# Kernel tuning notes

Hardware: AMD Instinct MI355X
Metric: run time of the kernel (lower is better)

## Reference

```python
import jax, jax.numpy as jnp
import numpy as np

UNITS = 128
N_CLASSES = 10
N_FEAT = 3
R_ON = 0.05      # time-gate open ratio
ALPHA = 0.001    # leak during closed phase
LN_EPS = 1e-3    # keras LayerNormalization default epsilon


def _time_gate(t, tau, s):
    # t: [B], tau/s: [U] -> k: [B, U]
    phi = jnp.mod(t[:, None] - s, tau) / tau
    k = jnp.where(phi < 0.5 * R_ON, 2.0 * phi / R_ON,
        jnp.where(phi < R_ON, 2.0 - 2.0 * phi / R_ON, ALPHA * phi))
    return k


def _plstm_step(x, t, h, c, Wx, Wh, b, tau, s):
    z = x @ Wx + h @ Wh + b                      # [B, 4U]
    i, f, g, o = jnp.split(z, 4, axis=-1)
    c_hat = jax.nn.sigmoid(f) * c + jax.nn.sigmoid(i) * jnp.tanh(g)
    h_hat = jax.nn.sigmoid(o) * jnp.tanh(c_hat)
    k = _time_gate(t, tau, s)
    return k * h_hat + (1.0 - k) * h, k * c_hat + (1.0 - k) * c


def _layer_norm(x, gamma, beta):
    mu = jnp.mean(x, axis=-1, keepdims=True)
    var = jnp.mean(jnp.square(x - mu), axis=-1, keepdims=True)
    return gamma * (x - mu) * jax.lax.rsqrt(var + LN_EPS) + beta


def setup_inputs() -> dict:
    key = jax.random.key(0)
    ks = jax.random.split(key, 16)
    B, T, F, U, C = 256, 1000, N_FEAT, UNITS, N_CLASSES
    inputs = jax.random.normal(ks[0], (B, T, F), dtype=jnp.float32)
    # strictly increasing-ish observation times per sequence
    times = jnp.cumsum(jax.random.uniform(ks[1], (B, T), dtype=jnp.float32), axis=1)
    sc_in = 1.0 / np.sqrt(F)
    sc_h = 1.0 / np.sqrt(U)
    Wx0 = jax.random.normal(ks[2], (F, 4 * U), dtype=jnp.float32) * sc_in
    Wh0 = jax.random.normal(ks[3], (U, 4 * U), dtype=jnp.float32) * sc_h
    b0 = jnp.zeros((4 * U,), dtype=jnp.float32)
    tau0 = jnp.exp(jax.random.uniform(ks[4], (U,), minval=0.0, maxval=3.0, dtype=jnp.float32))
    s0 = jax.random.uniform(ks[5], (U,), dtype=jnp.float32) * tau0
    Wx1 = jax.random.normal(ks[6], (U, 4 * U), dtype=jnp.float32) * sc_h
    Wh1 = jax.random.normal(ks[7], (U, 4 * U), dtype=jnp.float32) * sc_h
    b1 = jnp.zeros((4 * U,), dtype=jnp.float32)
    tau1 = jnp.exp(jax.random.uniform(ks[8], (U,), minval=0.0, maxval=3.0, dtype=jnp.float32))
    s1 = jax.random.uniform(ks[9], (U,), dtype=jnp.float32) * tau1
    gamma = jnp.ones((U,), dtype=jnp.float32)
    beta = jnp.zeros((U,), dtype=jnp.float32)
    Wfc = jax.random.normal(ks[10], (U, C), dtype=jnp.float32) * sc_h
    bfc = jnp.zeros((C,), dtype=jnp.float32)
    return {"inputs": inputs, "times": times, "Wx0": Wx0, "Wh0": Wh0, "b0": b0,
            "tau0": tau0, "s0": s0, "Wx1": Wx1, "Wh1": Wh1, "b1": b1,
            "tau1": tau1, "s1": s1, "gamma": gamma, "beta": beta,
            "Wfc": Wfc, "bfc": bfc}


def reference(inputs, times, Wx0, Wh0, b0, tau0, s0, Wx1, Wh1, b1, tau1, s1,
              gamma, beta, Wfc, bfc):
    B, T, F = inputs.shape
    U = Wh0.shape[0]
    x_t = jnp.transpose(inputs, (1, 0, 2))   # [T, B, F]
    t_t = jnp.transpose(times, (1, 0))       # [T, B]

    def step(carry, xt):
        h0, c0, h1, c1 = carry
        x, t = xt
        h0, c0 = _plstm_step(x, t, h0, c0, Wx0, Wh0, b0, tau0, s0)
        hn = _layer_norm(h0, gamma, beta)
        h1, c1 = _plstm_step(hn, t, h1, c1, Wx1, Wh1, b1, tau1, s1)
        probs = jax.nn.softmax(h1 @ Wfc + bfc, axis=-1)
        return (h0, c0, h1, c1), probs

    zeros = jnp.zeros((B, U), dtype=inputs.dtype)
    init = (zeros, zeros, zeros, zeros)
    _, out = jax.lax.scan(step, init, (x_t, t_t))  # out: [T, B, C]
    return jnp.transpose(out, (1, 0, 2))           # [B, T, C]
```

## Files before the change

### kernel.cpp

```cpp
#include <hip/hip_runtime.h>
#include <math.h>

constexpr int U      = 128;
constexpr int G4     = 512;
constexpr int NCls   = 10;
constexpr int TSTEPS = 1000;
constexpr int BATCH  = 256;
constexpr int CROWS  = 48;


__device__ __forceinline__ float sigm(float x) {
    return 1.0f / (1.0f + __expf(-x));
}

__device__ __forceinline__ float tgate(float t, float tau, float s) {
    float r = fmodf(t - s, tau);
    if (r < 0.0f) r += tau;
    const float phi = r / tau;
    return (phi < 0.025f) ? 40.0f * phi
         : (phi < 0.05f)  ? 2.0f - 40.0f * phi
         : 0.001f * phi;
}

#define ROW4(WP, I, HB) { \
    float4 w_; \
    w_ = (WP)[((I)+0)*128]; ac.x += (HB).x*w_.x; ac.y += (HB).x*w_.y; ac.z += (HB).x*w_.z; ac.w += (HB).x*w_.w; \
    w_ = (WP)[((I)+1)*128]; ac.x += (HB).y*w_.x; ac.y += (HB).y*w_.y; ac.z += (HB).y*w_.z; ac.w += (HB).y*w_.w; \
    w_ = (WP)[((I)+2)*128]; ac.x += (HB).z*w_.x; ac.y += (HB).z*w_.y; ac.z += (HB).z*w_.z; ac.w += (HB).z*w_.w; \
    w_ = (WP)[((I)+3)*128]; ac.x += (HB).w*w_.x; ac.y += (HB).w*w_.y; ac.z += (HB).w*w_.z; ac.w += (HB).w*w_.w; }

__global__ __launch_bounds__(1024, 1) void plstm_fused(
    const float* __restrict__ inputs,
    const float* __restrict__ times,
    const float* __restrict__ Wx0,
    const float* __restrict__ Wh0,
    const float* __restrict__ b0,
    const float* __restrict__ tau0,
    const float* __restrict__ s0,
    const float* __restrict__ Wx1,
    const float* __restrict__ Wh1,
    const float* __restrict__ b1,
    const float* __restrict__ tau1,
    const float* __restrict__ s1,
    const float* __restrict__ gamma_,
    const float* __restrict__ beta_,
    const float* __restrict__ Wfc,
    const float* __restrict__ bfc,
    float* __restrict__ out)
{
    const int tid = threadIdx.x;
    const int c4  = tid & 127;
    const int g   = tid >> 7;
    const int b   = blockIdx.x;

    __shared__ __align__(16) float wh0c[CROWS * G4];
    __shared__ __align__(16) float zu[8 * G4];
    __shared__ __align__(16) float h0s[U];
    __shared__ __align__(16) float ghu[2 * U];
    __shared__ __align__(16) float b0s[G4], b1s[G4], Ps[G4], Qs[G4];
    __shared__ __align__(16) float wx0s[3 * G4];
    __shared__ __align__(16) float wfcs[U * 11];
    __shared__ float bfcs[NCls];
    __shared__ float red[4];
    __shared__ float gms[U], bts[U];

    if (tid < U) { gms[tid] = gamma_[tid]; bts[tid] = beta_[tid];
                   h0s[tid] = 0.f; ghu[tid] = 0.f; ghu[U + tid] = 0.f; }
    {
        float4* dst = reinterpret_cast<float4*>(wh0c);
        const float4* src = reinterpret_cast<const float4*>(Wh0);
        #pragma unroll
        for (int i = 0; i < 6; ++i) dst[tid + i * 1024] = src[tid + i * 1024];
    }
    if (tid < G4) { b0s[tid] = b0[tid]; b1s[tid] = b1[tid]; }
    for (int i = tid; i < 3 * G4; i += 1024) wx0s[i] = Wx0[i];
    for (int i = tid; i < U * NCls; i += 1024) {
        const int u = i / NCls, c = i - u * NCls;
        wfcs[u * 11 + c] = Wfc[i];
    }
    if (tid < NCls) bfcs[tid] = bfc[tid];
    __syncthreads();

    if (tid < G4) {
        float P = 0.f, Q = 0.f;
        #pragma unroll 8
        for (int u = 0; u < U; ++u) {
            const float w = Wx1[u * G4 + tid];
            Q += gms[u] * w;
            P += bts[u] * w;
        }
        Ps[tid] = P; Qs[tid] = Q;
    }

    float tau0r = 0.f, s0r = 0.f, tau1r = 0.f, s1r = 0.f, gr = 0.f;
    if (tid < U) {
        tau0r = tau0[tid]; s0r = s0[tid];
        tau1r = tau1[tid]; s1r = s1[tid];
        gr = gms[tid];
    }
    float c0r = 0.f, c1r = 0.f, h0r = 0.f, h1r = 0.f;

    const float* __restrict__ xp = inputs + (size_t)b * TSTEPS * 3;
    const float* __restrict__ tp = times  + (size_t)b * TSTEPS;
    float*       __restrict__ op = out    + (size_t)b * TSTEPS * NCls;

    float xa0 = xp[0], xa1 = xp[1], xa2 = xp[2], tva = tp[0];

    __syncthreads();

    for (int t = 0; t < TSTEPS; ++t) {
        const float x0 = xa0, x1 = xa1, x2 = xa2, tv = tva;
        const int tn = (t + 1 < TSTEPS) ? t + 1 : t;
        xa0 = xp[tn*3+0]; xa1 = xp[tn*3+1]; xa2 = xp[tn*3+2]; tva = tp[tn];

        {
            float4 ac = make_float4(0.f, 0.f, 0.f, 0.f);
            const int r0 = g * 16;
            if (g < 3) {
                const float4* wp = reinterpret_cast<const float4*>(wh0c) + r0 * 128 + c4;
                #pragma unroll 2
                for (int i = 0; i < 16; i += 4) {
                    const float4 hb = *reinterpret_cast<const float4*>(&h0s[r0 + i]);
                    ROW4(wp, i, hb);
                }
            } else {
                const float4* wp = reinterpret_cast<const float4*>(Wh0) + r0 * 128 + c4;
                #pragma unroll 2
                for (int i = 0; i < 16; i += 4) {
                    const float4 hb = *reinterpret_cast<const float4*>(&h0s[r0 + i]);
                    ROW4(wp, i, hb);
                }
            }
            *reinterpret_cast<float4*>(&zu[g * G4 + 4 * c4]) = ac;
        }
        __syncthreads();

        if (tid < U) {
            const int u = tid;
            float z[4];
            #pragma unroll
            for (int q = 0; q < 4; ++q) {
                const int c = u + q * 128;
                float s = b0s[c] + x0 * wx0s[c] + x1 * wx0s[G4 + c] + x2 * wx0s[2 * G4 + c];
                #pragma unroll
                for (int gg = 0; gg < 8; ++gg) s += zu[gg * G4 + c];
                z[q] = s;
            }
            const float ig = sigm(z[0]);
            const float fg = sigm(z[1]);
            const float gg = tanhf(z[2]);
            const float og = sigm(z[3]);
            const float ch = fg * c0r + ig * gg;
            const float hh = og * tanhf(ch);
            const float k  = tgate(tv, tau0r, s0r);
            const float hn = k * hh + (1.0f - k) * h0r;
            c0r = k * ch + (1.0f - k) * c0r;
            h0r = hn;
            h0s[u] = hn;
            ghu[u] = gr * hn;
            float ssum = hn, qsum = hn * hn;
            #pragma unroll
            for (int off = 1; off < 64; off <<= 1) {
                ssum += __shfl_xor(ssum, off);
                qsum += __shfl_xor(qsum, off);
            }
            if ((tid & 63) == 0) {
                red[(tid >> 6) * 2]     = ssum;
                red[(tid >> 6) * 2 + 1] = qsum;
            }
        }
        __syncthreads();

        {
            const int half = tid >> 9;
            const int rg   = (tid >> 7) & 3;
            const int r0   = rg * 32;
            const float* __restrict__ Wm = half ? Wh1 : Wx1;
            const float* hvp = ghu + half * U + r0;
            const float4* wp = reinterpret_cast<const float4*>(Wm) + r0 * 128 + c4;
            float4 ac = make_float4(0.f, 0.f, 0.f, 0.f);
            #pragma unroll 2
            for (int i = 0; i < 32; i += 4) {
                const float4 hb = *reinterpret_cast<const float4*>(&hvp[i]);
                ROW4(wp, i, hb);
            }
            *reinterpret_cast<float4*>(&zu[(half * 4 + rg) * G4 + 4 * c4]) = ac;
        }
        __syncthreads();

        if (tid < U) {
            const float mu    = (red[0] + red[2]) * (1.0f / 128.0f);
            const float msq   = (red[1] + red[3]) * (1.0f / 128.0f);
            const float rstd  = rsqrtf(msq - mu * mu + 1e-3f);
            const float murstd = mu * rstd;
            const int u = tid;
            float z[4];
            #pragma unroll
            for (int q = 0; q < 4; ++q) {
                const int c = u + q * 128;
                const float sx = (zu[0*G4+c] + zu[1*G4+c]) + (zu[2*G4+c] + zu[3*G4+c]);
                const float sh = (zu[4*G4+c] + zu[5*G4+c]) + (zu[6*G4+c] + zu[7*G4+c]);
                z[q] = b1s[c] + Ps[c] + rstd * sx - murstd * Qs[c] + sh;
            }
            const float ig = sigm(z[0]);
            const float fg = sigm(z[1]);
            const float gg = tanhf(z[2]);
            const float og = sigm(z[3]);
            const float ch = fg * c1r + ig * gg;
            const float hh = og * tanhf(ch);
            const float k  = tgate(tv, tau1r, s1r);
            const float hn = k * hh + (1.0f - k) * h1r;
            c1r = k * ch + (1.0f - k) * c1r;
            h1r = hn;
            ghu[U + u] = hn;
        }
        __syncthreads();

        if (tid < 64) {
            const float a  = ghu[U + tid];
            const float bv = ghu[U + tid + 64];
            float p[NCls];
            #pragma unroll
            for (int c = 0; c < NCls; ++c)
                p[c] = a * wfcs[tid * 11 + c] + bv * wfcs[(tid + 64) * 11 + c];
            #pragma unroll
            for (int off = 1; off < 64; off <<= 1) {
                #pragma unroll
                for (int c = 0; c < NCls; ++c) p[c] += __shfl_xor(p[c], off);
            }
            float m = -1e30f;
            #pragma unroll
            for (int c = 0; c < NCls; ++c) { p[c] += bfcs[c]; m = fmaxf(m, p[c]); }
            float ssum = 0.0f;
            #pragma unroll
            for (int c = 0; c < NCls; ++c) { p[c] = __expf(p[c] - m); ssum += p[c]; }
            const float inv = 1.0f / ssum;
            float pv = p[0];
            #pragma unroll
            for (int c = 1; c < NCls; ++c) if (tid == c) pv = p[c];
            if (tid < NCls) op[t * NCls + tid] = pv * inv;
        }
    }
}

extern "C" void kernel_launch(void* const* d_in, const int* in_sizes, int n_in,
                              void* d_out, int out_size, void* d_ws, size_t ws_size,
                              hipStream_t stream) {
    const float* inputs = (const float*)d_in[0];
    const float* times  = (const float*)d_in[1];
    const float* Wx0    = (const float*)d_in[2];
    const float* Wh0    = (const float*)d_in[3];
    const float* b0     = (const float*)d_in[4];
    const float* tau0   = (const float*)d_in[5];
    const float* s0     = (const float*)d_in[6];
    const float* Wx1    = (const float*)d_in[7];
    const float* Wh1    = (const float*)d_in[8];
    const float* b1     = (const float*)d_in[9];
    const float* tau1   = (const float*)d_in[10];
    const float* s1     = (const float*)d_in[11];
    const float* gamma_ = (const float*)d_in[12];
    const float* beta_  = (const float*)d_in[13];
    const float* Wfc    = (const float*)d_in[14];
    const float* bfc    = (const float*)d_in[15];
    float* out = (float*)d_out;

    dim3 grid(BATCH);
    dim3 block(1024);
    hipLaunchKernelGGL(plstm_fused, grid, block, 0, stream,
                       inputs, times, Wx0, Wh0, b0, tau0, s0,
                       Wx1, Wh1, b1, tau1, s1, gamma_, beta_, Wfc, bfc, out);
}
```

Before: 7.087 ms.

## Halve block size and keep part of recurrent weights in registers

The block shrinks from 1024 to 512 threads. Each thread now holds 12 rows of Wh0 and 4 rows of Wx1/Wh1 as float4 registers. The rest of Wh0 is split between shared memory and global/L2 streaming, and the layer-1 matvec is regrouped into 4 partial sums instead of 8, which cuts the number of partial-sum reductions. Time-gate parameters move to shared memory to save registers. The aim is less shared and global weight traffic per timestep, at the cost of more serial FMA work per thread and higher register pressure with half the threads.

Measured after the change: 6.842 ms. 3.5% less time.

```diff
diff --git a/kernel.cpp b/kernel.cpp
--- a/kernel.cpp
+++ b/kernel.cpp
@@ -6,7 +6,6 @@
 constexpr int NCls   = 10;
 constexpr int TSTEPS = 1000;
 constexpr int BATCH  = 256;
-constexpr int CROWS  = 48;
 
 
 __device__ __forceinline__ float sigm(float x) {
@@ -29,7 +28,13 @@
     w_ = (WP)[((I)+2)*128]; ac.x += (HB).z*w_.x; ac.y += (HB).z*w_.y; ac.z += (HB).z*w_.z; ac.w += (HB).z*w_.w; \
     w_ = (WP)[((I)+3)*128]; ac.x += (HB).w*w_.x; ac.y += (HB).w*w_.y; ac.z += (HB).w*w_.z; ac.w += (HB).w*w_.w; }
 
-__global__ __launch_bounds__(1024, 1) void plstm_fused(
+#define ROW4P(W0, W1, W2, W3, HB) { \
+    ac.x += (HB).x*(W0).x; ac.y += (HB).x*(W0).y; ac.z += (HB).x*(W0).z; ac.w += (HB).x*(W0).w; \
+    ac.x += (HB).y*(W1).x; ac.y += (HB).y*(W1).y; ac.z += (HB).y*(W1).z; ac.w += (HB).y*(W1).w; \
+    ac.x += (HB).z*(W2).x; ac.y += (HB).z*(W2).y; ac.z += (HB).z*(W2).z; ac.w += (HB).z*(W2).w; \
+    ac.x += (HB).w*(W3).x; ac.y += (HB).w*(W3).y; ac.z += (HB).w*(W3).z; ac.w += (HB).w*(W3).w; }
+
+__global__ __launch_bounds__(512, 1) void plstm_fused(
     const float* __restrict__ inputs,
     const float* __restrict__ times,
     const float* __restrict__ Wx0,
@@ -53,35 +58,48 @@
     const int g   = tid >> 7;
     const int b   = blockIdx.x;
 
-    __shared__ __align__(16) float wh0c[CROWS * G4];
-    __shared__ __align__(16) float zu[8 * G4];
+    __shared__ __align__(16) float wh0c[48 * G4];
+    __shared__ __align__(16) float zuA[4 * G4];
+    __shared__ __align__(16) float zuB[4 * G4];
     __shared__ __align__(16) float h0s[U];
     __shared__ __align__(16) float ghu[2 * U];
     __shared__ __align__(16) float b0s[G4], b1s[G4], Ps[G4], Qs[G4];
     __shared__ __align__(16) float wx0s[3 * G4];
     __shared__ __align__(16) float wfcs[U * 11];
+    __shared__ float tau0s[U], s0s[U], tau1s[U], s1s[U];
     __shared__ float bfcs[NCls];
     __shared__ float red[4];
     __shared__ float gms[U], bts[U];
 
-    if (tid < U) { gms[tid] = gamma_[tid]; bts[tid] = beta_[tid];
-                   h0s[tid] = 0.f; ghu[tid] = 0.f; ghu[U + tid] = 0.f; }
+    if (tid < U) {
+        gms[tid] = gamma_[tid]; bts[tid] = beta_[tid];
+        tau0s[tid] = tau0[tid]; s0s[tid] = s0[tid];
+        tau1s[tid] = tau1[tid]; s1s[tid] = s1[tid];
+        h0s[tid] = 0.f; ghu[tid] = 0.f; ghu[U + tid] = 0.f;
+    }
     {
         float4* dst = reinterpret_cast<float4*>(wh0c);
-        const float4* src = reinterpret_cast<const float4*>(Wh0);
         #pragma unroll
-        for (int i = 0; i < 6; ++i) dst[tid + i * 1024] = src[tid + i * 1024];
+        for (int i = 0; i < 12; ++i) {
+            const int idx  = i * 512 + tid;
+            const int slot = idx >> 7;
+            const int cq   = idx & 127;
+            const int grp  = slot / 12;
+            const int row  = 32 * grp + 12 + (slot - grp * 12);
+            dst[slot * 128 + cq] =
+                *reinterpret_cast<const float4*>(&Wh0[row * G4 + 4 * cq]);
+        }
     }
     if (tid < G4) { b0s[tid] = b0[tid]; b1s[tid] = b1[tid]; }
-    for (int i = tid; i < 3 * G4; i += 1024) wx0s[i] = Wx0[i];
-    for (int i = tid; i < U * NCls; i += 1024) {
+    for (int i = tid; i < 3 * G4; i += 512) wx0s[i] = Wx0[i];
+    for (int i = tid; i < U * NCls; i += 512) {
         const int u = i / NCls, c = i - u * NCls;
         wfcs[u * 11 + c] = Wfc[i];
     }
     if (tid < NCls) bfcs[tid] = bfc[tid];
     __syncthreads();
 
-    if (tid < G4) {
+    {
         float P = 0.f, Q = 0.f;
         #pragma unroll 8
         for (int u = 0; u < U; ++u) {
@@ -92,13 +110,26 @@
         Ps[tid] = P; Qs[tid] = Q;
     }
 
-    float tau0r = 0.f, s0r = 0.f, tau1r = 0.f, s1r = 0.f, gr = 0.f;
-    if (tid < U) {
-        tau0r = tau0[tid]; s0r = s0[tid];
-        tau1r = tau1[tid]; s1r = s1[tid];
-        gr = gms[tid];
-    }
-    float c0r = 0.f, c1r = 0.f, h0r = 0.f, h1r = 0.f;
+    float4 wh0r[12];
+    #pragma unroll
+    for (int i = 0; i < 12; ++i)
+        wh0r[i] = *reinterpret_cast<const float4*>(&Wh0[(32 * g + i) * G4 + 4 * c4]);
+    const float* __restrict__ Wc = (g < 2) ? Wx1 : Wh1;
+    const int rb = 64 * (g & 1);
+    float4 wcr[4];
+    #pragma unroll
+    for (int i = 0; i < 4; ++i)
+        wcr[i] = *reinterpret_cast<const float4*>(&Wc[(rb + i) * G4 + 4 * c4]);
+
+    float c0r = 0.f, h0r = 0.f, c1r = 0.f, h1r = 0.f;
+
+    const float4* __restrict__ wlA =
+        reinterpret_cast<const float4*>(wh0c) + (12 * g) * 128 + c4;
+    const float4* __restrict__ wsA =
+        reinterpret_cast<const float4*>(Wh0) + (32 * g + 24) * 128 + c4;
+    const float4* __restrict__ wsC =
+        reinterpret_cast<const float4*>(Wc) + (rb + 4) * 128 + c4;
+    const float* __restrict__ hvC = ghu + 64 * g;
 
     const float* __restrict__ xp = inputs + (size_t)b * TSTEPS * 3;
     const float* __restrict__ tp = times  + (size_t)b * TSTEPS;
@@ -115,23 +146,25 @@
 
         {
             float4 ac = make_float4(0.f, 0.f, 0.f, 0.f);
-            const int r0 = g * 16;
-            if (g < 3) {
-                const float4* wp = reinterpret_cast<const float4*>(wh0c) + r0 * 128 + c4;
-                #pragma unroll 2
-                for (int i = 0; i < 16; i += 4) {
-                    const float4 hb = *reinterpret_cast<const float4*>(&h0s[r0 + i]);
-                    ROW4(wp, i, hb);
-                }
-            } else {
-                const float4* wp = reinterpret_cast<const float4*>(Wh0) + r0 * 128 + c4;
-                #pragma unroll 2
-                for (int i = 0; i < 16; i += 4) {
-                    const float4 hb = *reinterpret_cast<const float4*>(&h0s[r0 + i]);
-                    ROW4(wp, i, hb);
-                }
-            }
-            *reinterpret_cast<float4*>(&zu[g * G4 + 4 * c4]) = ac;
+            {
+                const float4 hb0 = *reinterpret_cast<const float4*>(&h0s[32 * g + 0]);
+                ROW4P(wh0r[0], wh0r[1], wh0r[2], wh0r[3], hb0);
+                const float4 hb1 = *reinterpret_cast<const float4*>(&h0s[32 * g + 4]);
+                ROW4P(wh0r[4], wh0r[5], wh0r[6], wh0r[7], hb1);
+                const float4 hb2 = *reinterpret_cast<const float4*>(&h0s[32 * g + 8]);
+                ROW4P(wh0r[8], wh0r[9], wh0r[10], wh0r[11], hb2);
+            }
+            #pragma unroll
+            for (int i = 0; i < 12; i += 4) {
+                const float4 hb = *reinterpret_cast<const float4*>(&h0s[32 * g + 12 + i]);
+                ROW4(wlA, i, hb);
+            }
+            #pragma unroll
+            for (int i = 0; i < 8; i += 4) {
+                const float4 hb = *reinterpret_cast<const float4*>(&h0s[32 * g + 24 + i]);
+                ROW4(wsA, i, hb);
+            }
+            *reinterpret_cast<float4*>(&zuA[g * G4 + 4 * c4]) = ac;
         }
         __syncthreads();
 
@@ -142,22 +175,19 @@
             for (int q = 0; q < 4; ++q) {
                 const int c = u + q * 128;
                 float s = b0s[c] + x0 * wx0s[c] + x1 * wx0s[G4 + c] + x2 * wx0s[2 * G4 + c];
-                #pragma unroll
-                for (int gg = 0; gg < 8; ++gg) s += zu[gg * G4 + c];
+                s += (zuA[c] + zuA[G4 + c]) + (zuA[2 * G4 + c] + zuA[3 * G4 + c]);
                 z[q] = s;
             }
-            const float ig = sigm(z[0]);
-            const float fg = sigm(z[1]);
-            const float gg = tanhf(z[2]);
-            const float og = sigm(z[3]);
+            const float ig = sigm(z[0]), fg = sigm(z[1]);
+            const float gg = tanhf(z[2]), og = sigm(z[3]);
             const float ch = fg * c0r + ig * gg;
             const float hh = og * tanhf(ch);
-            const float k  = tgate(tv, tau0r, s0r);
+            const float k  = tgate(tv, tau0s[u], s0s[u]);
             const float hn = k * hh + (1.0f - k) * h0r;
             c0r = k * ch + (1.0f - k) * c0r;
             h0r = hn;
             h0s[u] = hn;
-            ghu[u] = gr * hn;
+            ghu[u] = gms[u] * hn;
             float ssum = hn, qsum = hn * hn;
             #pragma unroll
             for (int off = 1; off < 64; off <<= 1) {
@@ -172,19 +202,17 @@
         __syncthreads();
 
         {
-            const int half = tid >> 9;
-            const int rg   = (tid >> 7) & 3;
-            const int r0   = rg * 32;
-            const float* __restrict__ Wm = half ? Wh1 : Wx1;
-            const float* hvp = ghu + half * U + r0;
-            const float4* wp = reinterpret_cast<const float4*>(Wm) + r0 * 128 + c4;
             float4 ac = make_float4(0.f, 0.f, 0.f, 0.f);
-            #pragma unroll 2
-            for (int i = 0; i < 32; i += 4) {
-                const float4 hb = *reinterpret_cast<const float4*>(&hvp[i]);
-                ROW4(wp, i, hb);
-            }
-            *reinterpret_cast<float4*>(&zu[(half * 4 + rg) * G4 + 4 * c4]) = ac;
+            {
+                const float4 hb = *reinterpret_cast<const float4*>(&hvC[0]);
+                ROW4P(wcr[0], wcr[1], wcr[2], wcr[3], hb);
+            }
+            #pragma unroll 5
+            for (int i = 0; i < 60; i += 4) {
+                const float4 hb = *reinterpret_cast<const float4*>(&hvC[4 + i]);
+                ROW4(wsC, i, hb);
+            }
+            *reinterpret_cast<float4*>(&zuB[g * G4 + 4 * c4]) = ac;
         }
         __syncthreads();
 
@@ -198,17 +226,15 @@
             #pragma unroll
             for (int q = 0; q < 4; ++q) {
                 const int c = u + q * 128;
-                const float sx = (zu[0*G4+c] + zu[1*G4+c]) + (zu[2*G4+c] + zu[3*G4+c]);
-                const float sh = (zu[4*G4+c] + zu[5*G4+c]) + (zu[6*G4+c] + zu[7*G4+c]);
+                const float sx = zuB[c] + zuB[G4 + c];
+                const float sh = zuB[2 * G4 + c] + zuB[3 * G4 + c];
                 z[q] = b1s[c] + Ps[c] + rstd * sx - murstd * Qs[c] + sh;
             }
-            const float ig = sigm(z[0]);
-            const float fg = sigm(z[1]);
-            const float gg = tanhf(z[2]);
-            const float og = sigm(z[3]);
+            const float ig = sigm(z[0]), fg = sigm(z[1]);
+            const float gg = tanhf(z[2]), og = sigm(z[3]);
             const float ch = fg * c1r + ig * gg;
             const float hh = og * tanhf(ch);
-            const float k  = tgate(tv, tau1r, s1r);
+            const float k  = tgate(tv, tau1s[u], s1s[u]);
             const float hn = k * hh + (1.0f - k) * h1r;
             c1r = k * ch + (1.0f - k) * c1r;
             h1r = hn;
@@ -265,7 +291,7 @@
     float* out = (float*)d_out;
 
     dim3 grid(BATCH);
-    dim3 block(1024);
+    dim3 block(512);
     hipLaunchKernelGGL(plstm_fused, grid, block, 0, stream,
                        inputs, times, Wx0, Wh0, b0, tau0, s0,
                        Wx1, Wh1, b1, tau1, s1, gamma_, beta_, Wfc, bfc, out);
```
